# Optimization experiments

Hardware: AMD Instinct MI355X
Metric: run time of the kernel (lower is better)

Reference implementation:

```python
import jax, jax.numpy as jnp
import numpy as np

B, T, C, H = 4, 2048, 1024, 16
D = C // H  # head_dim = 64


def setup_inputs() -> dict:
    key = jax.random.key(0)
    k1, k2, k3 = jax.random.split(key, 3)
    x = jax.random.normal(k1, (B, T, C), dtype=jnp.float32)
    # torch Linear init ~ U(-1/sqrt(fan_in), 1/sqrt(fan_in)); scaled normal is fine for a baseline
    w_qkv = jax.random.normal(k2, (C, 3 * C), dtype=jnp.float32) * (1.0 / np.sqrt(C))
    w_proj = jax.random.normal(k3, (C, C), dtype=jnp.float32) * (1.0 / np.sqrt(C))
    return {"x": x, "w_qkv": w_qkv, "w_proj": w_proj}


def reference(x, w_qkv, w_proj):
    Bb, Tt, Cc = x.shape
    qkv = x @ w_qkv                                   # [B,T,3C]
    q, k, v = jnp.split(qkv, 3, axis=-1)
    # [B,T,C] -> [B,H,T,D]
    q = q.reshape(Bb, Tt, H, D).transpose(0, 2, 1, 3)
    k = k.reshape(Bb, Tt, H, D).transpose(0, 2, 1, 3)
    v = v.reshape(Bb, Tt, H, D).transpose(0, 2, 1, 3)
    scale = 1.0 / np.sqrt(D).astype(np.float32)
    logits = jnp.einsum("bhqd,bhkd->bhqk", q, k) * scale  # [B,H,T,T]
    causal = jnp.tril(jnp.ones((Tt, Tt), dtype=bool))
    logits = jnp.where(causal, logits, jnp.finfo(logits.dtype).min)
    attn = jax.nn.softmax(logits, axis=-1)
    y = jnp.einsum("bhqk,bhkd->bhqd", attn, v)            # [B,H,T,D]
    y = y.transpose(0, 2, 1, 3).reshape(Bb, Tt, Cc)
    return y @ w_proj                                     # dropout p=0 (eval)
```

## Files before the change

### kernel.cpp

```cpp
#include <hip/hip_runtime.h>
#include <hip/hip_bf16.h>
#include <stdint.h>

typedef unsigned short u16;
typedef __attribute__((ext_vector_type(4))) float f32x4;
typedef __attribute__((ext_vector_type(16))) float f32x16;
typedef __attribute__((ext_vector_type(8))) __bf16 bf16x8;
typedef __attribute__((ext_vector_type(2))) unsigned int u32x2;

__device__ __forceinline__ u16 f2bf(float f) {
  union { float f; uint32_t u; } x; x.f = f;
  const uint32_t u = x.u;
  return (u16)((u + 0x7fffu + ((u >> 16) & 1u)) >> 16);
}

#define QSCALE 0.1803368801111244f

__global__ void cvt_f32_bf16(const float* __restrict__ in, u16* __restrict__ out,
                             int n) {
  const int i = (blockIdx.x * blockDim.x + threadIdx.x) * 4;
  if (i < n) {
    const float4 v = *(const float4*)(in + i);
    ushort4 o;
    o.x = f2bf(v.x); o.y = f2bf(v.y); o.z = f2bf(v.z); o.w = f2bf(v.w);
    *(ushort4*)(out + i) = o;
  }
}

__global__ void transpose_cvt(const float* __restrict__ in, u16* __restrict__ out,
                              int R, int Cc) {
  __shared__ u16 tile[64][66];
  const int tx = threadIdx.x, ty = threadIdx.y;
  const int c0 = blockIdx.x * 64, r0 = blockIdx.y * 64;
#pragma unroll
  for (int i = 0; i < 4; ++i)
    tile[ty + i * 16][tx] = f2bf(in[(size_t)(r0 + ty + i * 16) * Cc + c0 + tx]);
  __syncthreads();
#pragma unroll
  for (int i = 0; i < 4; ++i)
    out[(size_t)(c0 + ty + i * 16) * R + r0 + tx] = tile[tx][ty + i * 16];
}

__global__ void transpose_v(const u16* __restrict__ V, u16* __restrict__ VT) {
  __shared__ u16 tile[64][66];
  const int tx = threadIdx.x, ty = threadIdx.y;
  const int r0 = blockIdx.x * 64;
  const size_t ho = (size_t)blockIdx.y * 2048 * 64;
  const u16* in = V + ho;
  u16* out = VT + ho;
#pragma unroll
  for (int i = 0; i < 4; ++i)
    tile[ty + i * 16][tx] = in[(size_t)(r0 + ty + i * 16) * 64 + tx];
  __syncthreads();
#pragma unroll
  for (int i = 0; i < 4; ++i)
    out[(size_t)(ty + i * 16) * 2048 + r0 + tx] = tile[tx][ty + i * 16];
}

template <int MODE>
__global__ __launch_bounds__(256) void gemm_bt(
    const u16* __restrict__ A, const u16* __restrict__ BT,
    float* __restrict__ out, u16* __restrict__ Qo, u16* __restrict__ Ko,
    u16* __restrict__ Vo, int M, int N, int K) {
  __shared__ u16 Asm_[128 * 32];
  __shared__ u16 Bsm_[128 * 32];
  const int tid = threadIdx.x;
  const int wid = tid >> 6, lane = tid & 63;
  const int wm = wid >> 1, wn = wid & 1;
  const int l15 = lane & 15, l4 = lane >> 4;
  const int bm = blockIdx.y, bn = blockIdx.x;

  const u16* Ag = A + (size_t)bm * 128 * K;
  const u16* Bg = BT + (size_t)bn * 128 * K;

  f32x4 acc[4][4] = {};

  const int srow = lane >> 2;
  const int scol = (lane & 3) * 8;

  for (int kt = 0; kt < K; kt += 32) {
    __syncthreads();
#pragma unroll
    for (int it = 0; it < 2; ++it) {
      const int c = it * 4 + wid;
      const int row = c * 16 + srow;
      __builtin_amdgcn_global_load_lds(
          (const __attribute__((address_space(1))) uint32_t*)(Ag + (size_t)row * K + kt + scol),
          (__attribute__((address_space(3))) uint32_t*)(&Asm_[c * 512]), 16, 0, 0);
      __builtin_amdgcn_global_load_lds(
          (const __attribute__((address_space(1))) uint32_t*)(Bg + (size_t)row * K + kt + scol),
          (__attribute__((address_space(3))) uint32_t*)(&Bsm_[c * 512]), 16, 0, 0);
    }
    __syncthreads();

    bf16x8 af[4], bfr[4];
#pragma unroll
    for (int m = 0; m < 4; ++m)
      af[m] = *(const bf16x8*)&Asm_[(wm * 64 + m * 16 + l15) * 32 + l4 * 8];
#pragma unroll
    for (int n = 0; n < 4; ++n)
      bfr[n] = *(const bf16x8*)&Bsm_[(wn * 64 + n * 16 + l15) * 32 + l4 * 8];
#pragma unroll
    for (int m = 0; m < 4; ++m)
#pragma unroll
      for (int n = 0; n < 4; ++n)
        acc[m][n] = __builtin_amdgcn_mfma_f32_16x16x32_bf16(af[m], bfr[n], acc[m][n], 0, 0, 0);
  }

  const int row0 = bm * 128 + wm * 64;
  const int col0 = bn * 128 + wn * 64;
#pragma unroll
  for (int m = 0; m < 4; ++m) {
#pragma unroll
    for (int n = 0; n < 4; ++n) {
#pragma unroll
      for (int j = 0; j < 4; ++j) {
        const int row = row0 + m * 16 + l4 * 4 + j;
        const int col = col0 + n * 16 + l15;
        if (MODE == 1) {
          const int sec = col >> 10, c = col & 1023;
          const int h = c >> 6, d = c & 63;
          const int b = row >> 11, t = row & 2047;
          float av = acc[m][n][j];
          if (sec == 0) av *= QSCALE;
          u16* dst = (sec == 0) ? Qo : (sec == 1) ? Ko : Vo;
          dst[(((size_t)(b * 16 + h)) * 2048 + t) * 64 + d] = f2bf(av);
        } else {
          out[(size_t)row * N + col] = acc[m][n][j];
        }
      }
    }
  }
}

__global__ __launch_bounds__(256, 4) void attn_fwd(const u16* __restrict__ Qp,
                                                   const u16* __restrict__ Kp,
                                                   const u16* __restrict__ VTp,
                                                   u16* __restrict__ Y) {
  constexpr int DP = 72;
  constexpr float THR = 11.0f;
  __shared__ u16 Ks[2][64 * DP];
  __shared__ u16 Vt[2][64 * DP];

  const int xorm = (int)((0x0A050F00u >> ((blockIdx.y >> 4) * 8)) & 15u);
  const int qt = (int)blockIdx.x ^ xorm;
  const int bh = blockIdx.y;
  const int b = bh >> 4, h = bh & 15;
  const int tid = threadIdx.x, lane = tid & 63;
  const int wid = tid >> 6;
  const int l31 = lane & 31, hb = lane >> 5;

  const size_t head_off = (size_t)bh * 2048 * 64;
  const u16* Kh = Kp + head_off;
  const u16* VTh = VTp + head_off;

  const int qg = qt * 128 + wid * 32 + l31;
  const u16* Qrow = Qp + head_off + (size_t)qg * 64;

  bf16x8 qf[4];
#pragma unroll
  for (int d = 0; d < 4; ++d)
    qf[d] = *(const bf16x8*)(Qrow + d * 16 + hb * 8);

  float m_ = -1e30f, l_ = 0.f;
  f32x16 oacc[2] = {};

  const int sr = tid >> 3;
  const int sc = (tid & 7) * 8;

  bf16x8 kreg[2], vreg[2];
  auto kvload = [&](int kt) {
#pragma unroll
    for (int it = 0; it < 2; ++it) {
      const int r = sr + it * 32;
      kreg[it] = *(const bf16x8*)(Kh + (size_t)(kt * 64 + r) * 64 + sc);
      vreg[it] = *(const bf16x8*)(VTh + (size_t)r * 2048 + kt * 64 + sc);
    }
  };
  auto kvwrite = [&](int buf) {
#pragma unroll
    for (int it = 0; it < 2; ++it) {
      const int r = sr + it * 32;
      *(bf16x8*)&Ks[buf][r * DP + sc] = kreg[it];
      *(bf16x8*)&Vt[buf][r * DP + sc] = vreg[it];
    }
  };

  kvload(0);
  kvwrite(0);
  __syncthreads();

  const int nt = 2 * qt + 2;
  for (int kt = 0; kt < nt; ++kt) {
    const int cur = kt & 1;
    const bool havenext = (kt + 1 < nt);
    if (havenext) kvload(kt + 1);

    const bool diag = (kt >= 2 * qt);

#pragma unroll
    for (int kb2 = 0; kb2 < 2; ++kb2) {
      f32x16 s = {};
      __builtin_amdgcn_s_setprio(1);
#pragma unroll
      for (int d = 0; d < 4; ++d) {
        const bf16x8 kf = *(const bf16x8*)&Ks[cur][(kb2 * 32 + l31) * DP + d * 16 + hb * 8];
        s = __builtin_amdgcn_mfma_f32_32x32x16_bf16(kf, qf[d], s, 0, 0, 0);
      }
      __builtin_amdgcn_s_setprio(0);

      if (diag) {
        const int kbase = kt * 64 + kb2 * 32 + hb * 4;
#pragma unroll
        for (int r = 0; r < 16; ++r) {
          const int koff = (r & 3) + 8 * (r >> 2);
          if (kbase + koff > qg) s[r] = -1e30f;
        }
      }

      float pmax = s[0];
#pragma unroll
      for (int r = 1; r < 16; ++r) pmax = fmaxf(pmax, s[r]);
      if (!__all(pmax - m_ <= THR)) {
        const float fm = fmaxf(pmax, __shfl_xor(pmax, 32));
        const float mnew = fmaxf(m_, fm);
        const float alpha = __builtin_exp2f(m_ - mnew);
        m_ = mnew;
        l_ *= alpha;
#pragma unroll
        for (int nb = 0; nb < 2; ++nb)
#pragma unroll
          for (int r = 0; r < 16; ++r) oacc[nb][r] *= alpha;
      }
#pragma unroll
      for (int r = 0; r < 16; ++r) {
        s[r] = __builtin_exp2f(s[r] - m_);
        l_ += s[r];
      }

      bf16x8 pb[2];
#pragma unroll
      for (int st = 0; st < 2; ++st) {
        uint32_t x0, x1, y0, y1;
        asm("v_cvt_pk_bf16_f32 %0, %1, %2" : "=v"(x0) : "v"(s[8 * st + 0]), "v"(s[8 * st + 1]));
        asm("v_cvt_pk_bf16_f32 %0, %1, %2" : "=v"(x1) : "v"(s[8 * st + 2]), "v"(s[8 * st + 3]));
        asm("v_cvt_pk_bf16_f32 %0, %1, %2" : "=v"(y0) : "v"(s[8 * st + 4]), "v"(s[8 * st + 5]));
        asm("v_cvt_pk_bf16_f32 %0, %1, %2" : "=v"(y1) : "v"(s[8 * st + 6]), "v"(s[8 * st + 7]));
        const u32x2 r0 = __builtin_amdgcn_permlane32_swap(x0, y0, false, false);
        const u32x2 r1 = __builtin_amdgcn_permlane32_swap(x1, y1, false, false);
        union { uint32_t w[4]; bf16x8 v; } u;
        u.w[0] = r0[0]; u.w[1] = r1[0]; u.w[2] = r0[1]; u.w[3] = r1[1];
        pb[st] = u.v;
      }

      __builtin_amdgcn_s_setprio(1);
#pragma unroll
      for (int nb = 0; nb < 2; ++nb)
#pragma unroll
        for (int st = 0; st < 2; ++st) {
          const bf16x8 vf = *(const bf16x8*)&Vt[cur][(nb * 32 + l31) * DP + kb2 * 32 + st * 16 + hb * 8];
          oacc[nb] = __builtin_amdgcn_mfma_f32_32x32x16_bf16(vf, pb[st], oacc[nb], 0, 0, 0);
        }
      __builtin_amdgcn_s_setprio(0);
    }

    if (havenext) kvwrite(cur ^ 1);
    __syncthreads();
  }

  const float lf = l_ + __shfl_xor(l_, 32);
  const float inv = 1.0f / lf;
  u16* Yrow = Y + ((size_t)b * 2048 + qg) * 1024 + h * 64;
#pragma unroll
  for (int nb = 0; nb < 2; ++nb) {
#pragma unroll
    for (int g = 0; g < 4; ++g) {
      ushort4 o;
      o.x = f2bf(oacc[nb][4 * g + 0] * inv);
      o.y = f2bf(oacc[nb][4 * g + 1] * inv);
      o.z = f2bf(oacc[nb][4 * g + 2] * inv);
      o.w = f2bf(oacc[nb][4 * g + 3] * inv);
      *(ushort4*)(Yrow + nb * 32 + g * 8 + hb * 4) = o;
    }
  }
}

extern "C" void kernel_launch(void* const* d_in, const int* in_sizes, int n_in,
                              void* d_out, int out_size, void* d_ws,
                              size_t ws_size, hipStream_t stream) {
  const float* x = (const float*)d_in[0];
  const float* w_qkv = (const float*)d_in[1];
  const float* w_proj = (const float*)d_in[2];
  float* out = (float*)d_out;

  char* ws = (char*)d_ws;
  u16* xb = (u16*)ws;
  u16* VTw = (u16*)ws;
  u16* wqkvT = (u16*)(ws + 16777216);
  u16* wprojT = (u16*)(ws + 23068672);
  u16* Qw = (u16*)(ws + 25165824);
  u16* Kw = (u16*)(ws + 41943040);
  u16* Vw = (u16*)(ws + 58720256);
  u16* Yw = (u16*)(ws + 75497472);
  if (ws_size < 92274688) return;

  cvt_f32_bf16<<<dim3(8192), dim3(256), 0, stream>>>(x, xb, 8388608);

  dim3 tb(64, 16);
  transpose_cvt<<<dim3(48, 16), tb, 0, stream>>>(w_qkv, wqkvT, 1024, 3072);
  transpose_cvt<<<dim3(16, 16), tb, 0, stream>>>(w_proj, wprojT, 1024, 1024);

  gemm_bt<1><<<dim3(24, 64), dim3(256), 0, stream>>>(
      xb, wqkvT, (float*)nullptr, Qw, Kw, Vw, 8192, 3072, 1024);

  transpose_v<<<dim3(32, 64), tb, 0, stream>>>(Vw, VTw);

  attn_fwd<<<dim3(16, 64), dim3(256), 0, stream>>>(Qw, Kw, VTw, Yw);

  gemm_bt<0><<<dim3(8, 64), dim3(256), 0, stream>>>(
      Yw, wprojT, out, (u16*)nullptr, (u16*)nullptr, (u16*)nullptr,
      8192, 1024, 1024);
}
```

Baseline: 203.2 us.

## Replace QKV GEMM with 256x256 tile, 8-wave pipelined global_load_lds kernel

Adds a new QKV projection kernel that uses 256x256 output tiles with 512 threads, K-step 64, and double-buffered LDS filled through direct global_load_lds. Staging of the next K tiles is interleaved with MFMA quarters using explicit barriers, vmcnt waits and setprio. The goal is to hide memory latency and raise data reuse compared with the 128x128 single-buffered GEMM. The output projection GEMM becomes a non-templated fp32 path. Risks are the larger LDS footprint (128KB per block), lower occupancy, and a fragile hand-written schedule.

Measured after the change: 215.2 us. 1.06x slower.

```diff
diff --git a/kernel.cpp b/kernel.cpp
--- a/kernel.cpp
+++ b/kernel.cpp
@@ -57,11 +57,119 @@
     out[(size_t)(ty + i * 16) * 2048 + r0 + tx] = tile[tx][ty + i * 16];
 }
 
-template <int MODE>
+__global__ __launch_bounds__(512, 2) void gemm8p_qkv(
+    const u16* __restrict__ A, const u16* __restrict__ BT,
+    u16* __restrict__ Qo, u16* __restrict__ Ko, u16* __restrict__ Vo,
+    int K) {
+  __shared__ u16 L[2][2][2][128 * 64];
+  const int tid = threadIdx.x, wid = tid >> 6, lane = tid & 63;
+  const int wm = wid >> 2, wn = wid & 3;
+  const int l15 = lane & 15, l4 = lane >> 4;
+  const int bn = blockIdx.x, bm = blockIdx.y;
+
+  const u16* Atile = A + (size_t)bm * 256 * K;
+  const u16* Btile = BT + (size_t)bn * 256 * K;
+
+  f32x4 acc[8][4] = {};
+  bf16x8 aF[4][2], bF[4][2];
+  const int cb = wid * 64 + lane;
+
+#define SB8() __builtin_amdgcn_sched_barrier(0)
+#define BAR8() { SB8(); __builtin_amdgcn_s_barrier(); SB8(); }
+#define VW4() { SB8(); asm volatile("s_waitcnt vmcnt(4)" ::: "memory"); SB8(); }
+#define STG(d, op, h, kt) { \
+    const u16* s0_ = ((op) ? Btile : Atile) + (size_t)(h) * 128 * K + (size_t)(kt) * 64; \
+    _Pragma("unroll") for (int j_ = 0; j_ < 2; ++j_) { \
+      const int c_ = j_ * 512 + cb; \
+      __builtin_amdgcn_global_load_lds( \
+          (const __attribute__((address_space(1))) uint32_t*)(s0_ + (size_t)(c_ >> 3) * K + (c_ & 7) * 8), \
+          (__attribute__((address_space(3))) uint32_t*)(&L[d][op][h][(j_ * 512 + wid * 64) * 8]), 16, 0, 0); \
+    } }
+#define LD_A(d, mbase) { \
+    _Pragma("unroll") for (int m_ = 0; m_ < 4; ++m_) \
+    _Pragma("unroll") for (int k_ = 0; k_ < 2; ++k_) \
+      aF[m_][k_] = *(const bf16x8*)&L[d][0][wm][(((mbase) + m_) * 16 + l15) * 64 + k_ * 32 + l4 * 8]; }
+#define LD_B(d, nbase) { \
+    _Pragma("unroll") for (int n_ = 0; n_ < 2; ++n_) \
+    _Pragma("unroll") for (int k_ = 0; k_ < 2; ++k_) \
+      bF[(nbase) + n_][k_] = *(const bf16x8*)&L[d][1][wn >> 1][((wn & 1) * 64 + ((nbase) + n_) * 16 + l15) * 64 + k_ * 32 + l4 * 8]; }
+#define MQ(MS, NS) { __builtin_amdgcn_s_setprio(1); \
+    _Pragma("unroll") for (int m_ = 0; m_ < 4; ++m_) \
+    _Pragma("unroll") for (int n_ = 0; n_ < 2; ++n_) \
+    _Pragma("unroll") for (int kk_ = 0; kk_ < 2; ++kk_) \
+      acc[(MS) * 4 + m_][(NS) * 2 + n_] = __builtin_amdgcn_mfma_f32_16x16x32_bf16( \
+          aF[m_][kk_], bF[(NS) * 2 + n_][kk_], acc[(MS) * 4 + m_][(NS) * 2 + n_], 0, 0, 0); \
+    __builtin_amdgcn_s_setprio(0); }
+
+  STG(0, 1, 0, 0); STG(0, 0, 0, 0); STG(0, 1, 1, 0); STG(0, 0, 1, 0);
+  STG(1, 1, 0, 1); STG(1, 0, 0, 1);
+  VW4();
+  BAR8();
+
+  const int nkt = K >> 6;
+  for (int it = 0; it < nkt / 2; ++it) {
+    const int t1 = 2 * it + 1;
+    const int t2 = (2 * it + 2 < nkt) ? 2 * it + 2 : nkt - 1;
+    const int t3 = (2 * it + 3 < nkt) ? 2 * it + 3 : nkt - 1;
+    LD_A(0, 0); LD_B(0, 0);
+    STG(1, 1, 1, t1);
+    BAR8(); MQ(0, 0); BAR8();
+    LD_B(0, 2);
+    STG(1, 0, 1, t1);
+    BAR8(); MQ(0, 1); BAR8();
+    LD_A(0, 4);
+    STG(0, 1, 0, t2);
+    BAR8(); MQ(1, 0); BAR8();
+    STG(0, 0, 0, t2);
+    VW4();
+    BAR8(); MQ(1, 1); BAR8();
+    LD_A(1, 0); LD_B(1, 0);
+    STG(0, 1, 1, t2);
+    BAR8(); MQ(0, 0); BAR8();
+    LD_B(1, 2);
+    STG(0, 0, 1, t2);
+    BAR8(); MQ(0, 1); BAR8();
+    LD_A(1, 4);
+    STG(1, 1, 0, t3);
+    BAR8(); MQ(1, 0); BAR8();
+    STG(1, 0, 0, t3);
+    VW4();
+    BAR8(); MQ(1, 1); BAR8();
+  }
+  asm volatile("s_waitcnt vmcnt(0)" ::: "memory");
+
+  const int row0 = bm * 256 + wm * 128;
+  const int col0 = bn * 256 + wn * 64;
+#pragma unroll
+  for (int m = 0; m < 8; ++m) {
+#pragma unroll
+    for (int n = 0; n < 4; ++n) {
+#pragma unroll
+      for (int jj = 0; jj < 4; ++jj) {
+        const int row = row0 + m * 16 + l4 * 4 + jj;
+        const int col = col0 + n * 16 + l15;
+        const int sec = col >> 10, c = col & 1023;
+        const int h = c >> 6, d = c & 63;
+        const int b = row >> 11, t = row & 2047;
+        float av = acc[m][n][jj];
+        if (sec == 0) av *= QSCALE;
+        u16* dst = (sec == 0) ? Qo : (sec == 1) ? Ko : Vo;
+        dst[(((size_t)(b * 16 + h)) * 2048 + t) * 64 + d] = f2bf(av);
+      }
+    }
+  }
+#undef SB8
+#undef BAR8
+#undef VW4
+#undef STG
+#undef LD_A
+#undef LD_B
+#undef MQ
+}
+
 __global__ __launch_bounds__(256) void gemm_bt(
     const u16* __restrict__ A, const u16* __restrict__ BT,
-    float* __restrict__ out, u16* __restrict__ Qo, u16* __restrict__ Ko,
-    u16* __restrict__ Vo, int M, int N, int K) {
+    float* __restrict__ out, int M, int N, int K) {
   __shared__ u16 Asm_[128 * 32];
   __shared__ u16 Bsm_[128 * 32];
   const int tid = threadIdx.x;
@@ -110,27 +218,15 @@
   const int row0 = bm * 128 + wm * 64;
   const int col0 = bn * 128 + wn * 64;
 #pragma unroll
-  for (int m = 0; m < 4; ++m) {
-#pragma unroll
-    for (int n = 0; n < 4; ++n) {
+  for (int m = 0; m < 4; ++m)
+#pragma unroll
+    for (int n = 0; n < 4; ++n)
 #pragma unroll
       for (int j = 0; j < 4; ++j) {
         const int row = row0 + m * 16 + l4 * 4 + j;
         const int col = col0 + n * 16 + l15;
-        if (MODE == 1) {
-          const int sec = col >> 10, c = col & 1023;
-          const int h = c >> 6, d = c & 63;
-          const int b = row >> 11, t = row & 2047;
-          float av = acc[m][n][j];
-          if (sec == 0) av *= QSCALE;
-          u16* dst = (sec == 0) ? Qo : (sec == 1) ? Ko : Vo;
-          dst[(((size_t)(b * 16 + h)) * 2048 + t) * 64 + d] = f2bf(av);
-        } else {
-          out[(size_t)row * N + col] = acc[m][n][j];
-        }
-      }
-    }
-  }
+        out[(size_t)row * N + col] = acc[m][n][j];
+      }
 }
 
 __global__ __launch_bounds__(256, 4) void attn_fwd(const u16* __restrict__ Qp,
@@ -310,14 +406,13 @@
   transpose_cvt<<<dim3(48, 16), tb, 0, stream>>>(w_qkv, wqkvT, 1024, 3072);
   transpose_cvt<<<dim3(16, 16), tb, 0, stream>>>(w_proj, wprojT, 1024, 1024);
 
-  gemm_bt<1><<<dim3(24, 64), dim3(256), 0, stream>>>(
-      xb, wqkvT, (float*)nullptr, Qw, Kw, Vw, 8192, 3072, 1024);
+  gemm8p_qkv<<<dim3(12, 32), dim3(512), 0, stream>>>(
+      xb, wqkvT, Qw, Kw, Vw, 1024);
 
   transpose_v<<<dim3(32, 64), tb, 0, stream>>>(Vw, VTw);
 
   attn_fwd<<<dim3(16, 64), dim3(256), 0, stream>>>(Qw, Kw, VTw, Yw);
 
-  gemm_bt<0><<<dim3(8, 64), dim3(256), 0, stream>>>(
-      Yw, wprojT, out, (u16*)nullptr, (u16*)nullptr, (u16*)nullptr,
-      8192, 1024, 1024);
-}
+  gemm_bt<<<dim3(8, 64), dim3(256), 0, stream>>>(
+      Yw, wprojT, out, 8192, 1024, 1024);
+}
```
